# Kernel optimization log

Hardware: AMD Instinct MI355X
Metric: run time of the kernel (lower is better)

The kernel has to match this reference:

```python
import jax, jax.numpy as jnp
import numpy as np

B, N, C, H = 2, 2048, 768, 12
D = C // H  # head dim = 64


def _rotate_half(x):
    d2 = x.shape[-1] // 2
    x1, x2 = x[..., :d2], x[..., d2:]
    return jnp.concatenate([-x2, x1], axis=-1)


def _apply_rope(x, sin, cos):
    # x: [B,H,N,D], sin/cos: [N,D] -> broadcast over (B,H)
    return x * cos[None, None] + _rotate_half(x) * sin[None, None]


def setup_inputs() -> dict:
    key = jax.random.key(0)
    ks = jax.random.split(key, 7)
    x = jax.random.normal(ks[0], (B, N, C), dtype=jnp.float32)
    sin_spatial = jax.random.normal(ks[1], (N, D), dtype=jnp.float32)
    cos_spatial = jax.random.normal(ks[2], (N, D), dtype=jnp.float32)
    s = 1.0 / np.sqrt(C)
    W_qkv = jax.random.uniform(ks[3], (C, 3 * C), jnp.float32, -s, s)
    b_qkv = jax.random.uniform(ks[4], (3 * C,), jnp.float32, -s, s)
    W_out = jax.random.uniform(ks[5], (C, C), jnp.float32, -s, s)
    b_out = jax.random.uniform(ks[6], (C,), jnp.float32, -s, s)
    return {"x": x, "sin_spatial": sin_spatial, "cos_spatial": cos_spatial,
            "W_qkv": W_qkv, "b_qkv": b_qkv, "W_out": W_out, "b_out": b_out}


def reference(x, sin_spatial, cos_spatial, W_qkv, b_qkv, W_out, b_out):
    qkv = x @ W_qkv + b_qkv                       # [B,N,3C]
    qkv = qkv.reshape(B, N, 3, H, D).transpose(2, 0, 3, 1, 4)  # [3,B,H,N,D]
    q, k, v = qkv[0], qkv[1], qkv[2]
    q = _apply_rope(q, sin_spatial, cos_spatial)
    k = _apply_rope(k, sin_spatial, cos_spatial)
    att = jnp.einsum('bhqd,bhkd->bhqk', q, k) * (D ** -0.5)
    att = jax.nn.softmax(att, axis=-1)            # dropout is identity (eval)
    y = jnp.einsum('bhqk,bhkd->bhqd', att, v)     # [B,H,N,D]
    y = y.transpose(0, 2, 1, 3).reshape(B, N, C)
    return y @ W_out + b_out
```

## Files before the change

kernel.cpp:

```cpp
#include <hip/hip_runtime.h>
#include <hip/hip_bf16.h>

#define BB 2
#define NN 2048
#define CC 768
#define HH 12
#define DD 64
#define MM 4096
#define N3 2304

typedef __attribute__((ext_vector_type(8))) short bf16x8;
typedef __attribute__((ext_vector_type(4))) float f32x4;

#define QSCALE 0.18033688011112043f


__device__ __forceinline__ unsigned short f2bf(float f) {
    union { float f; unsigned u; } v; v.f = f;
    unsigned r = v.u + 0x7FFFu + ((v.u >> 16) & 1u);
    return (unsigned short)(r >> 16);
}

__device__ __forceinline__ short f2bf_rn(float f) {
    union { __hip_bfloat16 h; short s; } v;
    v.h = __float2bfloat16(f);
    return v.s;
}

__device__ __forceinline__ float exp2_hw(float x) {
    float r;
    asm("v_exp_f32 %0, %1" : "=v"(r) : "v"(x));
    return r;
}

__device__ __forceinline__ bf16x8 ld_frag(const unsigned short* p) {
    bf16x8 r;
    __builtin_memcpy(&r, p, 8);
    __builtin_memcpy((char*)&r + 8, p + 16, 8);
    return r;
}

__device__ __forceinline__ bf16x8 ld_frag16(const unsigned short* p) {
    bf16x8 r;
    __builtin_memcpy(&r, p, 16);
    return r;
}

__global__ void k_cvt(const float* __restrict__ s, unsigned short* __restrict__ d, int n4) {
    int i = blockIdx.x * blockDim.x + threadIdx.x;
    int st = gridDim.x * blockDim.x;
    for (; i < n4; i += st) {
        float4 v = ((const float4*)s)[i];
        ushort4 o;
        o.x = f2bf(v.x); o.y = f2bf(v.y); o.z = f2bf(v.z); o.w = f2bf(v.w);
        ((ushort4*)d)[i] = o;
    }
}

__global__ void k_cvtT(const float* __restrict__ s, unsigned short* __restrict__ d,
                       int R, int Cc) {
    __shared__ unsigned short t[64][72];
    const int c0 = blockIdx.x * 64, r0 = blockIdx.y * 64;
    const int tr = threadIdx.x >> 4;
    const int tc = (threadIdx.x & 15) * 4;
#pragma unroll
    for (int i = 0; i < 4; i++) {
        int r = tr + i * 16;
        float4 v = *(const float4*)(s + (size_t)(r0 + r) * Cc + c0 + tc);
        t[tc + 0][r] = f2bf(v.x);
        t[tc + 1][r] = f2bf(v.y);
        t[tc + 2][r] = f2bf(v.z);
        t[tc + 3][r] = f2bf(v.w);
    }
    __syncthreads();
    const int wr = threadIdx.x >> 2;
    const int wc = (threadIdx.x & 3) * 16;
    *(uint4*)(d + (size_t)(c0 + wr) * R + r0 + wc)     = *(uint4*)&t[wr][wc];
    *(uint4*)(d + (size_t)(c0 + wr) * R + r0 + wc + 8) = *(uint4*)&t[wr][wc + 8];
}

__launch_bounds__(256)
__global__ void k_qkv(const unsigned short* __restrict__ xb,
                      const unsigned short* __restrict__ wt,
                      const float* __restrict__ bias,
                      const float* __restrict__ sinp,
                      const float* __restrict__ cosp,
                      unsigned short* __restrict__ qws,
                      unsigned short* __restrict__ kws,
                      unsigned short* __restrict__ vws) {
    __shared__ unsigned short As[128][40];
    __shared__ unsigned short Bs[64][40];
    const int tid = threadIdx.x;
    const int lane = tid & 63, w = tid >> 6;
    const int ql = lane & 15, lg = lane >> 4;
    const int row0 = blockIdx.x * 128;
    const int j0 = blockIdx.y * 64;

    f32x4 acc[2][4];
#pragma unroll
    for (int a = 0; a < 2; a++)
#pragma unroll
        for (int b = 0; b < 4; b++) acc[a][b] = f32x4{0.f, 0.f, 0.f, 0.f};

    const int ar = tid >> 1, ac = (tid & 1) * 16;
    const int jr = tid >> 2, kc = (tid & 3) * 8;

    for (int k0 = 0; k0 < CC; k0 += 32) {
        uint4 av0 = *(const uint4*)(xb + (size_t)(row0 + ar) * CC + k0 + ac);
        uint4 av1 = *(const uint4*)(xb + (size_t)(row0 + ar) * CC + k0 + ac + 8);
        uint4 bv  = *(const uint4*)(wt + (size_t)(j0 + jr) * CC + k0 + kc);
        *(uint4*)&As[ar][ac]     = av0;
        *(uint4*)&As[ar][ac + 8] = av1;
        *(uint4*)&Bs[jr][kc]     = bv;
        __syncthreads();

        bf16x8 af[2], bfr[4];
#pragma unroll
        for (int fr = 0; fr < 2; fr++) af[fr] = ld_frag(&As[w * 32 + fr * 16 + ql][lg * 4]);
#pragma unroll
        for (int fn = 0; fn < 4; fn++) bfr[fn] = ld_frag(&Bs[fn * 16 + ql][lg * 4]);
#pragma unroll
        for (int fr = 0; fr < 2; fr++)
#pragma unroll
            for (int fn = 0; fn < 4; fn++)
                acc[fr][fn] = __builtin_amdgcn_mfma_f32_16x16x32_bf16(af[fr], bfr[fn], acc[fr][fn], 0, 0, 0);
        __syncthreads();
    }

    float vals[2][4][4];
#pragma unroll
    for (int fr = 0; fr < 2; fr++)
#pragma unroll
        for (int fn = 0; fn < 4; fn++) {
            float bj = bias[j0 + fn * 16 + ql];
#pragma unroll
            for (int r = 0; r < 4; r++) vals[fr][fn][r] = acc[fr][fn][r] + bj;
        }
    const int t = j0 / CC;
    const int h = (j0 % CC) >> 6;
    if (t < 2) {
        unsigned short* outp = (t == 0) ? qws : kws;
        const float qs = (t == 0) ? QSCALE : 1.0f;
#pragma unroll
        for (int fr = 0; fr < 2; fr++)
#pragma unroll
            for (int r = 0; r < 4; r++) {
                int m = row0 + w * 32 + fr * 16 + lg * 4 + r;
                int b = m >> 11, n = m & (NN - 1);
#pragma unroll
                for (int fn = 0; fn < 4; fn++) {
                    int d = fn * 16 + ql;
                    float cv = cosp[n * DD + d], sv = sinp[n * DD + d];
                    float other = vals[fr][fn ^ 2][r];
                    float rv = (vals[fr][fn][r] * cv + ((fn < 2) ? -other : other) * sv) * qs;
                    int dcol = (fn >> 1) * 32 + (ql >> 2) * 8 + (fn & 1) * 4 + (ql & 3);
                    outp[((size_t)(b * HH + h) * NN + n) * DD + dcol] = f2bf(rv);
                }
            }
    } else {
#pragma unroll
        for (int fr = 0; fr < 2; fr++)
#pragma unroll
            for (int r = 0; r < 4; r++) {
                int m = row0 + w * 32 + fr * 16 + lg * 4 + r;
                int b = m >> 11, n = m & (NN - 1);
                int ncol = (n & ~31) + lg * 8 + (fr & 1) * 4 + r;
#pragma unroll
                for (int fn = 0; fn < 4; fn++) {
                    int d = fn * 16 + ql;
                    vws[((size_t)(b * HH + h) * DD + d) * NN + ncol] = f2bf(vals[fr][fn][r]);
                }
            }
    }
}

__launch_bounds__(128)
__global__ void k_attn(const unsigned short* __restrict__ qws,
                       const unsigned short* __restrict__ kws,
                       const unsigned short* __restrict__ vws,
                       unsigned short* __restrict__ yws) {
    __shared__ unsigned short Ks[2][64][72];
    __shared__ unsigned short Vs[2][64][72];
    const int tid = threadIdx.x;
    const int lane = tid & 63, w = tid >> 6;
    const int ql = lane & 15, lg = lane >> 4;
    const int d0 = blockIdx.x;
    const int bh = (d0 & 7) + 8 * (d0 >> 8);
    const int qb = (d0 >> 3) & 31;
    const int qw = qb * 64 + w * 32;
    const unsigned short* Qp = qws + (size_t)bh * NN * DD;
    const unsigned short* Kp = kws + (size_t)bh * NN * DD;
    const unsigned short* Vp = vws + (size_t)bh * DD * NN;

    bf16x8 qf[2][2];
#pragma unroll
    for (int fn = 0; fn < 2; fn++)
#pragma unroll
        for (int kb = 0; kb < 2; kb++)
            qf[fn][kb] = ld_frag16(Qp + (size_t)(qw + fn * 16 + ql) * DD + kb * 32 + lg * 8);

    f32x4 oacc[4][2];
#pragma unroll
    for (int a = 0; a < 4; a++)
#pragma unroll
        for (int b = 0; b < 2; b++) oacc[a][b] = f32x4{0.f, 0.f, 0.f, 0.f};
    float mrun[2] = {-1e30f, -1e30f}, lrun[2] = {0.f, 0.f};

    const int srow = tid >> 1;
    const int shalf = (tid & 1) * 32;

#pragma unroll
    for (int j = 0; j < 4; j++) {
        *(uint4*)&Ks[0][srow][shalf + j * 8] = *(const uint4*)(Kp + (size_t)srow * DD + shalf + j * 8);
        *(uint4*)&Vs[0][srow][shalf + j * 8] = *(const uint4*)(Vp + (size_t)srow * NN + shalf + j * 8);
    }
    __syncthreads();

    const int NT = NN / 64;
    int cur = 0;
    for (int kt = 0; kt < NT; kt++) {
        uint4 kn[4], vn[4];
        const bool hasn = (kt + 1 < NT);
        if (hasn) {
#pragma unroll
            for (int j = 0; j < 4; j++) {
                kn[j] = *(const uint4*)(Kp + (size_t)((kt + 1) * 64 + srow) * DD + shalf + j * 8);
                vn[j] = *(const uint4*)(Vp + (size_t)srow * NN + (kt + 1) * 64 + shalf + j * 8);
            }
        }
        const unsigned short (*Kc)[72] = Ks[cur];
        const unsigned short (*Vc)[72] = Vs[cur];

        f32x4 sacc[4][2];
#pragma unroll
        for (int a = 0; a < 4; a++)
#pragma unroll
            for (int b = 0; b < 2; b++) sacc[a][b] = f32x4{0.f, 0.f, 0.f, 0.f};
        __builtin_amdgcn_s_setprio(1);
#pragma unroll
        for (int kb = 0; kb < 2; kb++) {
            bf16x8 kf[4];
#pragma unroll
            for (int fr = 0; fr < 4; fr++)
                kf[fr] = ld_frag16(&Kc[fr * 16 + ql][kb * 32 + lg * 8]);
#pragma unroll
            for (int fr = 0; fr < 4; fr++)
#pragma unroll
                for (int fn = 0; fn < 2; fn++)
                    sacc[fr][fn] = __builtin_amdgcn_mfma_f32_16x16x32_bf16(kf[fr], qf[fn][kb], sacc[fr][fn], 0, 0, 0);
        }
        __builtin_amdgcn_s_setprio(0);

        bf16x8 pB[2][2];
#pragma unroll
        for (int fn = 0; fn < 2; fn++) {
            float ma = fmaxf(fmaxf(sacc[0][fn][0], sacc[0][fn][1]), fmaxf(sacc[0][fn][2], sacc[0][fn][3]));
            float mb = fmaxf(fmaxf(sacc[1][fn][0], sacc[1][fn][1]), fmaxf(sacc[1][fn][2], sacc[1][fn][3]));
            float mc = fmaxf(fmaxf(sacc[2][fn][0], sacc[2][fn][1]), fmaxf(sacc[2][fn][2], sacc[2][fn][3]));
            float md = fmaxf(fmaxf(sacc[3][fn][0], sacc[3][fn][1]), fmaxf(sacc[3][fn][2], sacc[3][fn][3]));
            float tm = fmaxf(fmaxf(ma, mb), fmaxf(mc, md));
            tm = fmaxf(tm, __shfl_xor(tm, 16));
            tm = fmaxf(tm, __shfl_xor(tm, 32));
            if (__any(tm > mrun[fn] + 8.0f)) {
                float mn = fmaxf(mrun[fn], tm);
                float scl = exp2_hw(mrun[fn] - mn);
                lrun[fn] *= scl;
#pragma unroll
                for (int db = 0; db < 4; db++) oacc[db][fn] *= scl;
                mrun[fn] = mn;
            }
            float ts = 0.f;
#pragma unroll
            for (int fr = 0; fr < 4; fr++)
#pragma unroll
                for (int r = 0; r < 4; r++) {
                    float p = exp2_hw(sacc[fr][fn][r] - mrun[fn]);
                    sacc[fr][fn][r] = p;
                    ts += p;
                }
            ts += __shfl_xor(ts, 16);
            ts += __shfl_xor(ts, 32);
            lrun[fn] += ts;

#pragma unroll
            for (int kkb = 0; kkb < 2; kkb++) {
                bf16x8 t8;
#pragma unroll
                for (int e = 0; e < 8; e++)
                    t8[e] = f2bf_rn(sacc[kkb * 2 + (e >> 2)][fn][e & 3]);
                pB[fn][kkb] = t8;
            }
        }

        __builtin_amdgcn_s_setprio(1);
#pragma unroll
        for (int db = 0; db < 4; db++) {
            bf16x8 va[2];
#pragma unroll
            for (int kkb = 0; kkb < 2; kkb++)
                va[kkb] = ld_frag16(&Vc[db * 16 + ql][kkb * 32 + lg * 8]);
#pragma unroll
            for (int kkb = 0; kkb < 2; kkb++)
#pragma unroll
                for (int fn = 0; fn < 2; fn++)
                    oacc[db][fn] = __builtin_amdgcn_mfma_f32_16x16x32_bf16(va[kkb], pB[fn][kkb], oacc[db][fn], 0, 0, 0);
        }
        __builtin_amdgcn_s_setprio(0);

        if (hasn) {
#pragma unroll
            for (int j = 0; j < 4; j++) {
                *(uint4*)&Ks[cur ^ 1][srow][shalf + j * 8] = kn[j];
                *(uint4*)&Vs[cur ^ 1][srow][shalf + j * 8] = vn[j];
            }
            __syncthreads();
            cur ^= 1;
        }
    }

    const int b = bh / HH, h = bh % HH;
#pragma unroll
    for (int fn = 0; fn < 2; fn++) {
        float inv = 1.0f / lrun[fn];
        int q = qw + fn * 16 + ql;
        unsigned short* yp = yws + (size_t)(b * NN + q) * CC + h * DD + lg * 4;
#pragma unroll
        for (int db = 0; db < 4; db++) {
            ushort4 o;
            o.x = f2bf(oacc[db][fn][0] * inv);
            o.y = f2bf(oacc[db][fn][1] * inv);
            o.z = f2bf(oacc[db][fn][2] * inv);
            o.w = f2bf(oacc[db][fn][3] * inv);
            *(ushort4*)(yp + db * 16) = o;
        }
    }
}

__launch_bounds__(256)
__global__ void k_out(const unsigned short* __restrict__ yb,
                      const unsigned short* __restrict__ wt,
                      const float* __restrict__ bias,
                      float* __restrict__ out) {
    __shared__ unsigned short As[128][40];
    __shared__ unsigned short Bs[64][40];
    const int tid = threadIdx.x;
    const int lane = tid & 63, w = tid >> 6;
    const int ql = lane & 15, lg = lane >> 4;
    const int row0 = blockIdx.x * 128;
    const int j0 = blockIdx.y * 64;

    f32x4 acc[2][4];
#pragma unroll
    for (int a = 0; a < 2; a++)
#pragma unroll
        for (int b = 0; b < 4; b++) acc[a][b] = f32x4{0.f, 0.f, 0.f, 0.f};

    const int ar = tid >> 1, ac = (tid & 1) * 16;
    const int jr = tid >> 2, kc = (tid & 3) * 8;

    for (int k0 = 0; k0 < CC; k0 += 32) {
        uint4 av0 = *(const uint4*)(yb + (size_t)(row0 + ar) * CC + k0 + ac);
        uint4 av1 = *(const uint4*)(yb + (size_t)(row0 + ar) * CC + k0 + ac + 8);
        uint4 bv  = *(const uint4*)(wt + (size_t)(j0 + jr) * CC + k0 + kc);
        *(uint4*)&As[ar][ac]     = av0;
        *(uint4*)&As[ar][ac + 8] = av1;
        *(uint4*)&Bs[jr][kc]     = bv;
        __syncthreads();

        bf16x8 af[2], bfr[4];
#pragma unroll
        for (int fr = 0; fr < 2; fr++) af[fr] = ld_frag(&As[w * 32 + fr * 16 + ql][lg * 4]);
#pragma unroll
        for (int fn = 0; fn < 4; fn++) bfr[fn] = ld_frag(&Bs[fn * 16 + ql][lg * 4]);
#pragma unroll
        for (int fr = 0; fr < 2; fr++)
#pragma unroll
            for (int fn = 0; fn < 4; fn++)
                acc[fr][fn] = __builtin_amdgcn_mfma_f32_16x16x32_bf16(af[fr], bfr[fn], acc[fr][fn], 0, 0, 0);
        __syncthreads();
    }

#pragma unroll
    for (int fr = 0; fr < 2; fr++)
#pragma unroll
        for (int fn = 0; fn < 4; fn++) {
            float bj = bias[j0 + fn * 16 + ql];
#pragma unroll
            for (int r = 0; r < 4; r++) {
                int m = row0 + w * 32 + fr * 16 + lg * 4 + r;
                out[(size_t)m * CC + j0 + fn * 16 + ql] = acc[fr][fn][r] + bj;
            }
        }
}

extern "C" void kernel_launch(void* const* d_in, const int* in_sizes, int n_in,
                              void* d_out, int out_size, void* d_ws, size_t ws_size,
                              hipStream_t stream) {
    const float* x    = (const float*)d_in[0];
    const float* sinp = (const float*)d_in[1];
    const float* cosp = (const float*)d_in[2];
    const float* wqkv = (const float*)d_in[3];
    const float* bqkv = (const float*)d_in[4];
    const float* wout = (const float*)d_in[5];
    const float* bout = (const float*)d_in[6];
    float* out = (float*)d_out;
    char* ws = (char*)d_ws;

    unsigned short* xb  = (unsigned short*)(ws);
    unsigned short* wqb = (unsigned short*)(ws + 6291456);
    unsigned short* wob = (unsigned short*)(ws + 9830400);
    unsigned short* qws = (unsigned short*)(ws + 11010048);
    unsigned short* kws = (unsigned short*)(ws + 17301504);
    unsigned short* vws = (unsigned short*)(ws + 23592960);
    unsigned short* yws = (unsigned short*)(ws + 29884416);
    if (ws_size < 36175872) return;

    k_cvt<<<dim3(512), dim3(256), 0, stream>>>(x, xb, MM * CC / 4);
    k_cvtT<<<dim3(36, 12), dim3(256), 0, stream>>>(wqkv, wqb, CC, N3);
    k_cvtT<<<dim3(12, 12), dim3(256), 0, stream>>>(wout, wob, CC, CC);
    k_qkv<<<dim3(32, 36), dim3(256), 0, stream>>>(xb, wqb, bqkv, sinp, cosp, qws, kws, vws);
    k_attn<<<dim3(768), dim3(128), 0, stream>>>(qws, kws, vws, yws);
    k_out<<<dim3(32, 12), dim3(256), 0, stream>>>(yws, wob, bout, out);
}
```

Before: 135.7 us.

## Stage GEMM and attention tiles via direct global-to-LDS loads with permuted K layout

Replaces register-staged global-to-shared copies with async global_load_lds in the QKV GEMM, the out-projection GEMM, and the attention K/V tiles, and adds double buffering to both GEMMs. To let each lane read a contiguous 16-byte MFMA fragment, the conversion kernels and attention output now write bf16 data with the K dimension permuted within 32-element groups. Attention K/V tiles use an XOR swizzle in place of padding to avoid LDS bank conflicts, and K and V loading is split across the two waves. The aim is to cut VGPR pressure and load latency and to overlap fetches with MFMA work. The risk is that layout mismatches between producers and consumers, or waitcnt and synchronisation on the async loads, could break correctness.

```diff
diff --git a/kernel.cpp b/kernel.cpp
--- a/kernel.cpp
+++ b/kernel.cpp
@@ -33,17 +33,17 @@
     return r;
 }
 
-__device__ __forceinline__ bf16x8 ld_frag(const unsigned short* p) {
-    bf16x8 r;
-    __builtin_memcpy(&r, p, 8);
-    __builtin_memcpy((char*)&r + 8, p + 16, 8);
-    return r;
-}
-
 __device__ __forceinline__ bf16x8 ld_frag16(const unsigned short* p) {
     bf16x8 r;
     __builtin_memcpy(&r, p, 16);
     return r;
+}
+
+__device__ __forceinline__ void gload16(const unsigned short* g, unsigned short* l) {
+    __builtin_amdgcn_global_load_lds(
+        (const __attribute__((address_space(1))) void*)g,
+        (__attribute__((address_space(3))) void*)l,
+        16, 0, 0);
 }
 
 __global__ void k_cvt(const float* __restrict__ s, unsigned short* __restrict__ d, int n4) {
@@ -53,7 +53,9 @@
         float4 v = ((const float4*)s)[i];
         ushort4 o;
         o.x = f2bf(v.x); o.y = f2bf(v.y); o.z = f2bf(v.z); o.w = f2bf(v.w);
-        ((ushort4*)d)[i] = o;
+        int f = i * 4;
+        int dst = (f & ~31) + ((i & 3) << 3) + (((i >> 2) & 1) << 2);
+        *(ushort4*)(d + dst) = o;
     }
 }
 
@@ -75,8 +77,15 @@
     __syncthreads();
     const int wr = threadIdx.x >> 2;
     const int wc = (threadIdx.x & 3) * 16;
-    *(uint4*)(d + (size_t)(c0 + wr) * R + r0 + wc)     = *(uint4*)&t[wr][wc];
-    *(uint4*)(d + (size_t)(c0 + wr) * R + r0 + wc + 8) = *(uint4*)&t[wr][wc + 8];
+    unsigned short* drow = d + (size_t)(c0 + wr) * R + r0;
+#pragma unroll
+    for (int g = 0; g < 4; g++) {
+        int k4 = wc + g * 4;
+        int o = k4 & 31;
+        int p = (((o & 15) >> 2) << 3) + (((o >> 4) & 1) << 2);
+        ushort4 v4 = *(ushort4*)&t[wr][k4];
+        *(ushort4*)(drow + (k4 & ~31) + p) = v4;
+    }
 }
 
 __launch_bounds__(256)
@@ -88,8 +97,8 @@
                       unsigned short* __restrict__ qws,
                       unsigned short* __restrict__ kws,
                       unsigned short* __restrict__ vws) {
-    __shared__ unsigned short As[128][40];
-    __shared__ unsigned short Bs[64][40];
+    __shared__ unsigned short As[2][128 * 32];
+    __shared__ unsigned short Bs[2][64 * 32];
     const int tid = threadIdx.x;
     const int lane = tid & 63, w = tid >> 6;
     const int ql = lane & 15, lg = lane >> 4;
@@ -102,29 +111,38 @@
 #pragma unroll
         for (int b = 0; b < 4; b++) acc[a][b] = f32x4{0.f, 0.f, 0.f, 0.f};
 
-    const int ar = tid >> 1, ac = (tid & 1) * 16;
-    const int jr = tid >> 2, kc = (tid & 3) * 8;
-
+    const int sr = lane >> 2;
+    const int sc = (lane & 3) * 8;
+
+    auto stage = [&](int bi, int k0) {
+#pragma unroll
+        for (int c = 0; c < 2; c++) {
+            int j = w * 2 + c;
+            gload16(xb + (size_t)(row0 + j * 16 + sr) * CC + k0 + sc, &As[bi][j * 512]);
+        }
+        gload16(wt + (size_t)(j0 + w * 16 + sr) * CC + k0 + sc, &Bs[bi][w * 512]);
+    };
+
+    stage(0, 0);
+    __syncthreads();
+
+    int bufi = 0;
     for (int k0 = 0; k0 < CC; k0 += 32) {
-        uint4 av0 = *(const uint4*)(xb + (size_t)(row0 + ar) * CC + k0 + ac);
-        uint4 av1 = *(const uint4*)(xb + (size_t)(row0 + ar) * CC + k0 + ac + 8);
-        uint4 bv  = *(const uint4*)(wt + (size_t)(j0 + jr) * CC + k0 + kc);
-        *(uint4*)&As[ar][ac]     = av0;
-        *(uint4*)&As[ar][ac + 8] = av1;
-        *(uint4*)&Bs[jr][kc]     = bv;
-        __syncthreads();
-
+        if (k0 + 32 < CC) stage(bufi ^ 1, k0 + 32);
         bf16x8 af[2], bfr[4];
 #pragma unroll
-        for (int fr = 0; fr < 2; fr++) af[fr] = ld_frag(&As[w * 32 + fr * 16 + ql][lg * 4]);
-#pragma unroll
-        for (int fn = 0; fn < 4; fn++) bfr[fn] = ld_frag(&Bs[fn * 16 + ql][lg * 4]);
+        for (int fr = 0; fr < 2; fr++)
+            af[fr] = ld_frag16(&As[bufi][(w * 32 + fr * 16 + ql) * 32 + lg * 8]);
+#pragma unroll
+        for (int fn = 0; fn < 4; fn++)
+            bfr[fn] = ld_frag16(&Bs[bufi][(fn * 16 + ql) * 32 + lg * 8]);
 #pragma unroll
         for (int fr = 0; fr < 2; fr++)
 #pragma unroll
             for (int fn = 0; fn < 4; fn++)
                 acc[fr][fn] = __builtin_amdgcn_mfma_f32_16x16x32_bf16(af[fr], bfr[fn], acc[fr][fn], 0, 0, 0);
         __syncthreads();
+        bufi ^= 1;
     }
 
     float vals[2][4][4];
@@ -179,8 +197,8 @@
                        const unsigned short* __restrict__ kws,
                        const unsigned short* __restrict__ vws,
                        unsigned short* __restrict__ yws) {
-    __shared__ unsigned short Ks[2][64][72];
-    __shared__ unsigned short Vs[2][64][72];
+    __shared__ unsigned short Ksf[2][64 * 64];
+    __shared__ unsigned short Vsf[2][64 * 64];
     const int tid = threadIdx.x;
     const int lane = tid & 63, w = tid >> 6;
     const int ql = lane & 15, lg = lane >> 4;
@@ -206,30 +224,31 @@
         for (int b = 0; b < 2; b++) oacc[a][b] = f32x4{0.f, 0.f, 0.f, 0.f};
     float mrun[2] = {-1e30f, -1e30f}, lrun[2] = {0.f, 0.f};
 
-    const int srow = tid >> 1;
-    const int shalf = (tid & 1) * 32;
-
-#pragma unroll
-    for (int j = 0; j < 4; j++) {
-        *(uint4*)&Ks[0][srow][shalf + j * 8] = *(const uint4*)(Kp + (size_t)srow * DD + shalf + j * 8);
-        *(uint4*)&Vs[0][srow][shalf + j * 8] = *(const uint4*)(Vp + (size_t)srow * NN + shalf + j * 8);
-    }
+    const int sr8 = lane >> 3;
+    const int sun = (lane & 7) ^ sr8;
+
+    auto stageK = [&](int bi, int kt) {
+#pragma unroll
+        for (int j = 0; j < 8; j++)
+            gload16(Kp + (size_t)(kt * 64 + j * 8 + sr8) * DD + sun * 8, &Ksf[bi][j * 512]);
+    };
+    auto stageV = [&](int bi, int kt) {
+#pragma unroll
+        for (int j = 0; j < 8; j++)
+            gload16(Vp + (size_t)(j * 8 + sr8) * NN + kt * 64 + sun * 8, &Vsf[bi][j * 512]);
+    };
+
+    if (w == 0) stageK(0, 0); else stageV(0, 0);
     __syncthreads();
 
     const int NT = NN / 64;
     int cur = 0;
     for (int kt = 0; kt < NT; kt++) {
-        uint4 kn[4], vn[4];
-        const bool hasn = (kt + 1 < NT);
-        if (hasn) {
-#pragma unroll
-            for (int j = 0; j < 4; j++) {
-                kn[j] = *(const uint4*)(Kp + (size_t)((kt + 1) * 64 + srow) * DD + shalf + j * 8);
-                vn[j] = *(const uint4*)(Vp + (size_t)srow * NN + (kt + 1) * 64 + shalf + j * 8);
-            }
-        }
-        const unsigned short (*Kc)[72] = Ks[cur];
-        const unsigned short (*Vc)[72] = Vs[cur];
+        if (kt + 1 < NT) {
+            if (w == 0) stageK(cur ^ 1, kt + 1); else stageV(cur ^ 1, kt + 1);
+        }
+        const unsigned short* Kc = Ksf[cur];
+        const unsigned short* Vc = Vsf[cur];
 
         f32x4 sacc[4][2];
 #pragma unroll
@@ -242,7 +261,7 @@
             bf16x8 kf[4];
 #pragma unroll
             for (int fr = 0; fr < 4; fr++)
-                kf[fr] = ld_frag16(&Kc[fr * 16 + ql][kb * 32 + lg * 8]);
+                kf[fr] = ld_frag16(&Kc[(fr * 16 + ql) * 64 + (((kb * 4 + lg) ^ (ql & 7)) << 3)]);
 #pragma unroll
             for (int fr = 0; fr < 4; fr++)
 #pragma unroll
@@ -298,7 +317,7 @@
             bf16x8 va[2];
 #pragma unroll
             for (int kkb = 0; kkb < 2; kkb++)
-                va[kkb] = ld_frag16(&Vc[db * 16 + ql][kkb * 32 + lg * 8]);
+                va[kkb] = ld_frag16(&Vc[(db * 16 + ql) * 64 + (((kkb * 4 + lg) ^ (ql & 7)) << 3)]);
 #pragma unroll
             for (int kkb = 0; kkb < 2; kkb++)
 #pragma unroll
@@ -307,15 +326,8 @@
         }
         __builtin_amdgcn_s_setprio(0);
 
-        if (hasn) {
-#pragma unroll
-            for (int j = 0; j < 4; j++) {
-                *(uint4*)&Ks[cur ^ 1][srow][shalf + j * 8] = kn[j];
-                *(uint4*)&Vs[cur ^ 1][srow][shalf + j * 8] = vn[j];
-            }
-            __syncthreads();
-            cur ^= 1;
-        }
+        __syncthreads();
+        cur ^= 1;
     }
 
     const int b = bh / HH, h = bh % HH;
@@ -323,7 +335,7 @@
     for (int fn = 0; fn < 2; fn++) {
         float inv = 1.0f / lrun[fn];
         int q = qw + fn * 16 + ql;
-        unsigned short* yp = yws + (size_t)(b * NN + q) * CC + h * DD + lg * 4;
+        unsigned short* yp = yws + (size_t)(b * NN + q) * CC + h * DD;
 #pragma unroll
         for (int db = 0; db < 4; db++) {
             ushort4 o;
@@ -331,7 +343,7 @@
             o.y = f2bf(oacc[db][fn][1] * inv);
             o.z = f2bf(oacc[db][fn][2] * inv);
             o.w = f2bf(oacc[db][fn][3] * inv);
-            *(ushort4*)(yp + db * 16) = o;
+            *(ushort4*)(yp + (db >> 1) * 32 + lg * 8 + (db & 1) * 4) = o;
         }
     }
 }
@@ -341,8 +353,8 @@
                       const unsigned short* __restrict__ wt,
                       const float* __restrict__ bias,
                       float* __restrict__ out) {
-    __shared__ unsigned short As[128][40];
-    __shared__ unsigned short Bs[64][40];
+    __shared__ unsigned short As[2][128 * 32];
+    __shared__ unsigned short Bs[2][64 * 32];
     const int tid = threadIdx.x;
     const int lane = tid & 63, w = tid >> 6;
     const int ql = lane & 15, lg = lane >> 4;
@@ -355,29 +367,38 @@
 #pragma unroll
         for (int b = 0; b < 4; b++) acc[a][b] = f32x4{0.f, 0.f, 0.f, 0.f};
 
-    const int ar = tid >> 1, ac = (tid & 1) * 16;
-    const int jr = tid >> 2, kc = (tid & 3) * 8;
-
+    const int sr = lane >> 2;
+    const int sc = (lane & 3) * 8;
+
+    auto stage = [&](int bi, int k0) {
+#pragma unroll
+        for (int c = 0; c < 2; c++) {
+            int j = w * 2 + c;
+            gload16(yb + (size_t)(row0 + j * 16 + sr) * CC + k0 + sc, &As[bi][j * 512]);
+        }
+        gload16(wt + (size_t)(j0 + w * 16 + sr) * CC + k0 + sc, &Bs[bi][w * 512]);
+    };
+
+    stage(0, 0);
+    __syncthreads();
+
+    int bufi = 0;
     for (int k0 = 0; k0 < CC; k0 += 32) {
-        uint4 av0 = *(const uint4*)(yb + (size_t)(row0 + ar) * CC + k0 + ac);
-        uint4 av1 = *(const uint4*)(yb + (size_t)(row0 + ar) * CC + k0 + ac + 8);
-        uint4 bv  = *(const uint4*)(wt + (size_t)(j0 + jr) * CC + k0 + kc);
-        *(uint4*)&As[ar][ac]     = av0;
-        *(uint4*)&As[ar][ac + 8] = av1;
-        *(uint4*)&Bs[jr][kc]     = bv;
-        __syncthreads();
-
+        if (k0 + 32 < CC) stage(bufi ^ 1, k0 + 32);
         bf16x8 af[2], bfr[4];
 #pragma unroll
-        for (int fr = 0; fr < 2; fr++) af[fr] = ld_frag(&As[w * 32 + fr * 16 + ql][lg * 4]);
-#pragma unroll
-        for (int fn = 0; fn < 4; fn++) bfr[fn] = ld_frag(&Bs[fn * 16 + ql][lg * 4]);
+        for (int fr = 0; fr < 2; fr++)
+            af[fr] = ld_frag16(&As[bufi][(w * 32 + fr * 16 + ql) * 32 + lg * 8]);
+#pragma unroll
+        for (int fn = 0; fn < 4; fn++)
+            bfr[fn] = ld_frag16(&Bs[bufi][(fn * 16 + ql) * 32 + lg * 8]);
 #pragma unroll
         for (int fr = 0; fr < 2; fr++)
 #pragma unroll
             for (int fn = 0; fn < 4; fn++)
                 acc[fr][fn] = __builtin_amdgcn_mfma_f32_16x16x32_bf16(af[fr], bfr[fn], acc[fr][fn], 0, 0, 0);
         __syncthreads();
+        bufi ^= 1;
     }
 
 #pragma unroll
```

After: 141.4 us. 1.04x slower.
